# Kernel optimization log

Hardware: AMD Instinct MI355X
Metric: run time of the kernel (lower is better)

## Reference

```python
import jax, jax.numpy as jnp
import numpy as np

N = 100000   # nodes
E = 1600000  # edges (avg degree 16)
D = 128      # in_dim == out_dim (residual path)
NEG_SLOPE = 0.1


def setup_inputs() -> dict:
    key = jax.random.key(0)
    k1, k2, k3 = jax.random.split(key, 3)
    x = jax.random.normal(k1, (N, D), dtype=jnp.float32)
    edge_index = jax.random.randint(k2, (2, E), 0, N, dtype=jnp.int32)
    # GCNConv linear weight (stored as [in, out]; PyG uses x @ W^T with [out, in] — same math)
    W = jax.random.normal(k3, (D, D), dtype=jnp.float32) / np.sqrt(D).astype(np.float32)
    b = jnp.zeros((D,), dtype=jnp.float32)
    return {"x": x, "edge_index": edge_index, "W": W, "b": b}


def reference(x, edge_index, W, b):
    n = x.shape[0]
    # add self loops (GCNConv add_self_loops=True)
    loops = jnp.arange(n, dtype=edge_index.dtype)
    src = jnp.concatenate([edge_index[0], loops])
    dst = jnp.concatenate([edge_index[1], loops])
    # symmetric normalization: deg computed on destination index (PyG gcn_norm)
    deg = jax.ops.segment_sum(jnp.ones_like(dst, dtype=x.dtype), dst, num_segments=n)
    dinv = jnp.where(deg > 0, jax.lax.rsqrt(deg), 0.0)
    norm = dinv[src] * dinv[dst]                     # [E+N]
    # transform-then-propagate: small GEMM, then gather/scale/scatter
    h = x @ W                                        # [N, D]
    msgs = h[src] * norm[:, None]                    # [E+N, D] gather + scale
    agg = jax.ops.segment_sum(msgs, dst, num_segments=n) + b  # scatter-add
    act = jnp.where(agg >= 0, agg, NEG_SLOPE * agg)  # leaky_relu(0.1)
    return act + x                                   # residual (in_dim == out_dim)
```

## Files before the change

### kernel.cpp

```cpp
#include <hip/hip_runtime.h>
#include <hip/hip_bf16.h>

#define D 128
#define NEG_SLOPE 0.1f
#define BSHIFT 7
#define BSIZE 128
#define SRCBITS 17
#define SRCMASK 0x1FFFF
#define NBMAX 784
#define REGION 2432
#define EPBS 4096

typedef __attribute__((ext_vector_type(8))) short bf16x8;
typedef __attribute__((ext_vector_type(4))) float f32x4;
typedef __attribute__((ext_vector_type(2))) float f32x2;

__device__ inline unsigned short f2bf(float f) {
    unsigned u = __builtin_bit_cast(unsigned, f);
    u += 0x7fff + ((u >> 16) & 1);
    return (unsigned short)(u >> 16);
}

__global__ __launch_bounds__(256) void k_pre(const float* __restrict__ x, const float* __restrict__ W,
                                             const int* __restrict__ src, const int* __restrict__ dst,
                                             int* __restrict__ cursor, int* __restrict__ ebuf,
                                             unsigned char* __restrict__ h,
                                             int E, int NB, int n) {
    __shared__ __align__(16) unsigned char lds_u[34816];
    int b = blockIdx.x;
    int t = threadIdx.x;

    if (b < NB) {
        unsigned short* Wl = (unsigned short*)lds_u;
        const float4* W4 = (const float4*)W;
#pragma unroll
        for (int j = 0; j < 16; j++) {
            int e4 = j * 256 + t;
            float4 w = W4[e4];
            int e = e4 * 4;
            int k = e >> 7, n0 = e & 127;
            Wl[(n0 + 0) * 136 + k] = f2bf(w.x);
            Wl[(n0 + 1) * 136 + k] = f2bf(w.y);
            Wl[(n0 + 2) * 136 + k] = f2bf(w.z);
            Wl[(n0 + 3) * 136 + k] = f2bf(w.w);
        }
        __syncthreads();

        int lane = t & 63, wave = t >> 6;
        int quad = lane >> 4, mrow = lane & 15;
        int rbase = b * 128 + wave * 32;

        const float4* x4 = (const float4*)x;
        float4 a0[2][4], a1[2][4];
#pragma unroll
        for (int rt = 0; rt < 2; rt++) {
            int row = rbase + rt * 16 + mrow;
            long rowl = (row < n) ? row : (n - 1);
#pragma unroll
            for (int ks = 0; ks < 4; ks++) {
                long base = rowl * 32 + ks * 8 + quad * 2;
                a0[rt][ks] = x4[base];
                a1[rt][ks] = x4[base + 1];
            }
        }
        bf16x8 af[2][4];
#pragma unroll
        for (int rt = 0; rt < 2; rt++)
#pragma unroll
            for (int ks = 0; ks < 4; ks++) {
                bf16x8 f;
                f[0] = (short)f2bf(a0[rt][ks].x); f[1] = (short)f2bf(a0[rt][ks].y);
                f[2] = (short)f2bf(a0[rt][ks].z); f[3] = (short)f2bf(a0[rt][ks].w);
                f[4] = (short)f2bf(a1[rt][ks].x); f[5] = (short)f2bf(a1[rt][ks].y);
                f[6] = (short)f2bf(a1[rt][ks].z); f[7] = (short)f2bf(a1[rt][ks].w);
                af[rt][ks] = f;
            }

        f32x4 acc[2][8];
#pragma unroll
        for (int rt = 0; rt < 2; rt++)
#pragma unroll
            for (int ct = 0; ct < 8; ct++) acc[rt][ct] = (f32x4){0.f, 0.f, 0.f, 0.f};

#pragma unroll
        for (int ks = 0; ks < 4; ks++) {
#pragma unroll
            for (int ct = 0; ct < 8; ct++) {
                bf16x8 bf = *(bf16x8*)&Wl[(ct * 16 + mrow) * 136 + ks * 32 + quad * 8];
#pragma unroll
                for (int rt = 0; rt < 2; rt++)
                    acc[rt][ct] = __builtin_amdgcn_mfma_f32_16x16x32_bf16(af[rt][ks], bf, acc[rt][ct], 0, 0, 0);
            }
        }

#pragma unroll
        for (int rt = 0; rt < 2; rt++) {
#pragma unroll
            for (int reg = 0; reg < 4; reg++) {
                int row = rbase + rt * 16 + quad * 4 + reg;
                if (row < n) {
                    int w0 = __builtin_amdgcn_cvt_pk_fp8_f32(acc[rt][0][reg], acc[rt][1][reg], 0, false);
                    w0 = __builtin_amdgcn_cvt_pk_fp8_f32(acc[rt][2][reg], acc[rt][3][reg], w0, true);
                    int w1 = __builtin_amdgcn_cvt_pk_fp8_f32(acc[rt][4][reg], acc[rt][5][reg], 0, false);
                    w1 = __builtin_amdgcn_cvt_pk_fp8_f32(acc[rt][6][reg], acc[rt][7][reg], w1, true);
                    uint2 wv; wv.x = (unsigned)w0; wv.y = (unsigned)w1;
                    *(uint2*)&h[(long)row * 128 + mrow * 8] = wv;
                }
            }
        }
        return;
    }

    int sb = b - NB;
    int* cntL = (int*)lds_u;
    int* baseL = cntL + NBMAX;
    int* curL = baseL + NBMAX;
    for (int i = t; i < NB; i += 256) { cntL[i] = 0; }
    __syncthreads();

    const int4* src4 = (const int4*)src;
    const int4* dst4 = (const int4*)dst;
    int sv[16], dv[16];
#pragma unroll
    for (int j = 0; j < 4; j++) {
        int i4 = sb * 1024 + j * 256 + t;
        int e = i4 * 4;
        int4 s, d;
        if (e + 4 <= E) {
            s = src4[i4];
            d = dst4[i4];
        } else {
            s.x = (e < E) ? src[e] : 0;         d.x = (e < E) ? dst[e] : -1;
            s.y = (e + 1 < E) ? src[e + 1] : 0; d.y = (e + 1 < E) ? dst[e + 1] : -1;
            s.z = (e + 2 < E) ? src[e + 2] : 0; d.z = (e + 2 < E) ? dst[e + 2] : -1;
            s.w = (e + 3 < E) ? src[e + 3] : 0; d.w = (e + 3 < E) ? dst[e + 3] : -1;
        }
        sv[j * 4 + 0] = s.x; sv[j * 4 + 1] = s.y; sv[j * 4 + 2] = s.z; sv[j * 4 + 3] = s.w;
        dv[j * 4 + 0] = d.x; dv[j * 4 + 1] = d.y; dv[j * 4 + 2] = d.z; dv[j * 4 + 3] = d.w;
    }
#pragma unroll
    for (int k = 0; k < 16; k++)
        if (dv[k] >= 0) atomicAdd(&cntL[dv[k] >> BSHIFT], 1);
    __syncthreads();
    for (int i = t; i < NB; i += 256) {
        int c = cntL[i];
        if (c) baseL[i] = atomicAdd(&cursor[i], c);
        curL[i] = 0;
    }
    __syncthreads();
#pragma unroll
    for (int k = 0; k < 16; k++) {
        int d = dv[k];
        if (d >= 0) {
            int bk = d >> BSHIFT;
            int slot = baseL[bk] + atomicAdd(&curL[bk], 1);
            if (slot < REGION)
                ebuf[(long)bk * REGION + slot] = ((d & (BSIZE - 1)) << SRCBITS) | sv[k];
        }
    }
}

__global__ __launch_bounds__(256) void k_csr(const int* __restrict__ cursor, const int* __restrict__ ebuf,
                                             int* __restrict__ startA, int* __restrict__ degA,
                                             float* __restrict__ dinvA, int* __restrict__ sorted_src,
                                             int N) {
    __shared__ int srcL[REGION];
    __shared__ int cntL[BSIZE], startL[BSIZE], curL[BSIZE];

    int b = blockIdx.x, t = threadIdx.x;
    long estart = (long)b * REGION;
    int ecnt = cursor[b];
    if (ecnt > REGION) ecnt = REGION;

    if (t < BSIZE) cntL[t] = 0;
    __syncthreads();

    int ev[10];
#pragma unroll
    for (int k = 0; k < 10; k++) {
        int e = t + k * 256;
        ev[k] = (e < ecnt) ? ebuf[estart + e] : -1;
    }
#pragma unroll
    for (int k = 0; k < 10; k++)
        if (ev[k] >= 0) atomicAdd(&cntL[ev[k] >> SRCBITS], 1);
    __syncthreads();

    if (t < 64) {
        int d0 = cntL[2 * t], d1 = cntL[2 * t + 1];
        int sum = d0 + d1;
        int inc = sum;
        for (int sh = 1; sh < 64; sh <<= 1) {
            int y = __shfl_up(inc, sh, 64);
            if (t >= sh) inc += y;
        }
        int e0 = inc - sum;
        startL[2 * t] = e0;
        startL[2 * t + 1] = e0 + d0;
        curL[2 * t] = e0;
        curL[2 * t + 1] = e0 + d0;
    }
    __syncthreads();

    if (t < BSIZE) {
        int i = b * BSIZE + t;
        if (i < N) {
            startA[i] = b * REGION + startL[t];
            degA[i] = cntL[t];
            dinvA[i] = rsqrtf((float)cntL[t] + 1.0f);
        }
    }

#pragma unroll
    for (int k = 0; k < 10; k++)
        if (ev[k] >= 0) {
            int v = ev[k];
            int pos = atomicAdd(&curL[v >> SRCBITS], 1);
            srcL[pos] = v & SRCMASK;
        }
    __syncthreads();

    for (int e = t; e < ecnt; e += 256) sorted_src[estart + e] = srcL[e];
}

#define ACCVS(v, s)                                                           \
    {                                                                         \
        acc2[0] += __builtin_amdgcn_cvt_pk_f32_fp8((int)(v).x, false) * (s);  \
        acc2[1] += __builtin_amdgcn_cvt_pk_f32_fp8((int)(v).x, true) * (s);   \
        acc2[2] += __builtin_amdgcn_cvt_pk_f32_fp8((int)(v).y, false) * (s);  \
        acc2[3] += __builtin_amdgcn_cvt_pk_f32_fp8((int)(v).y, true) * (s);   \
        acc2[4] += __builtin_amdgcn_cvt_pk_f32_fp8((int)(v).z, false) * (s);  \
        acc2[5] += __builtin_amdgcn_cvt_pk_f32_fp8((int)(v).z, true) * (s);   \
        acc2[6] += __builtin_amdgcn_cvt_pk_f32_fp8((int)(v).w, false) * (s);  \
        acc2[7] += __builtin_amdgcn_cvt_pk_f32_fp8((int)(v).w, true) * (s);   \
    }

__global__ __launch_bounds__(256) void k_aggregate(const uint4* __restrict__ h4, const float* __restrict__ x,
                                                   const float* __restrict__ bias,
                                                   const int* __restrict__ startA, const int* __restrict__ degA,
                                                   const float* __restrict__ dinvA,
                                                   const int* __restrict__ sorted_src,
                                                   float* __restrict__ out, int n) {
    int wave = threadIdx.x >> 6, lane = threadIdx.x & 63;
    int i = blockIdx.x * 4 + wave;
    if (i >= n) return;
    int slot = lane >> 3, chunk = lane & 7;
    int start = startA[i], m = degA[i];
    float di = rsqrtf((float)m + 1.0f);

    f32x2 acc2[8];
#pragma unroll
    for (int r = 0; r < 8; r++) acc2[r] = (f32x2){0.f, 0.f};
    if (slot == 0) {
        uint4 v = h4[(long)i * 8 + chunk];
        ACCVS(v, di);
    }

    int j0 = 0;
    if (m >= 16) {
        int ja = start + slot;
        int e0 = sorted_src[ja], e1 = sorted_src[ja + 8];
        float dv0 = dinvA[e0], dv1 = dinvA[e1];
        for (;;) {
            uint4 v0 = h4[(long)e0 * 8 + chunk];
            uint4 v1 = h4[(long)e1 * 8 + chunk];
            j0 += 16;
            bool more = (j0 + 16 <= m);
            if (more) {
                int jb = start + j0 + slot;
                e0 = sorted_src[jb];
                e1 = sorted_src[jb + 8];
            }
            ACCVS(v0, dv0);
            ACCVS(v1, dv1);
            if (!more) break;
            dv0 = dinvA[e0];
            dv1 = dinvA[e1];
        }
    }
    if (j0 + 8 <= m) {
        int e = sorted_src[start + j0 + slot];
        float dv = dinvA[e];
        uint4 v = h4[(long)e * 8 + chunk];
        ACCVS(v, dv);
        j0 += 8;
    }
    for (int j = j0 + slot; j < m; j += 8) {
        int e = sorted_src[start + j];
        float dv = dinvA[e];
        uint4 v = h4[(long)e * 8 + chunk];
        ACCVS(v, dv);
    }

#pragma unroll
    for (int r = 0; r < 8; r++) {
        acc2[r].x += __shfl_xor(acc2[r].x, 8, 64);
        acc2[r].x += __shfl_xor(acc2[r].x, 16, 64);
        acc2[r].x += __shfl_xor(acc2[r].x, 32, 64);
        acc2[r].y += __shfl_xor(acc2[r].y, 8, 64);
        acc2[r].y += __shfl_xor(acc2[r].y, 16, 64);
        acc2[r].y += __shfl_xor(acc2[r].y, 32, 64);
    }

    int s1 = slot >> 1;
    f32x2 eL = (s1 == 0) ? acc2[0] : (s1 == 1) ? acc2[1] : (s1 == 2) ? acc2[2] : acc2[3];
    f32x2 eH = (s1 == 0) ? acc2[4] : (s1 == 1) ? acc2[5] : (s1 == 2) ? acc2[6] : acc2[7];
    float ax = (slot & 1) ? eL.y : eL.x;
    float ay = (slot & 1) ? eH.y : eH.x;

    int dbase = slot * 16 + chunk * 2;
    float2 bb = *(const float2*)&bias[dbase];
    float2 xv = *(const float2*)&x[(long)i * D + dbase];
    ax = ax * di + bb.x;
    ay = ay * di + bb.y;
    ax = (ax >= 0.f) ? ax : NEG_SLOPE * ax;
    ay = (ay >= 0.f) ? ay : NEG_SLOPE * ay;
    float2 o;
    o.x = ax + xv.x;
    o.y = ay + xv.y;
    *(float2*)&out[(long)i * D + dbase] = o;
}

extern "C" void kernel_launch(void* const* d_in, const int* in_sizes, int n_in,
                              void* d_out, int out_size, void* d_ws, size_t ws_size,
                              hipStream_t stream) {
    const float* x = (const float*)d_in[0];
    const int* edge_index = (const int*)d_in[1];
    const float* W = (const float*)d_in[2];
    const float* bias = (const float*)d_in[3];
    float* out = (float*)d_out;

    int N = in_sizes[0] / D;
    int E = in_sizes[1] / 2;
    const int* src = edge_index;
    const int* dst = edge_index + E;
    int NB = (N + BSIZE - 1) >> BSHIFT;
    int nbE = (E + EPBS - 1) / EPBS;

    char* ws = (char*)d_ws;
    size_t off = 0;
    auto alloc = [&](size_t bytes) {
        void* p = ws + off;
        off += (bytes + 15) & ~(size_t)15;
        return p;
    };
    int* cursor = (int*)alloc((size_t)NB * 4);
    int* ebuf = (int*)alloc((size_t)NB * REGION * 4);
    int* startA = (int*)alloc((size_t)N * 4);
    int* degA = (int*)alloc((size_t)N * 4);
    float* dinvA = (float*)alloc((size_t)N * 4);
    int* sorted_src = (int*)alloc((size_t)NB * REGION * 4);
    unsigned char* h = (unsigned char*)alloc((size_t)N * D);

    hipMemsetAsync(cursor, 0, (size_t)NB * 4, stream);
    k_pre<<<NB + nbE, 256, 0, stream>>>(x, W, src, dst, cursor, ebuf, h, E, NB, N);
    k_csr<<<NB, 256, 0, stream>>>(cursor, ebuf, startA, degA, dinvA, sorted_src, N);
    k_aggregate<<<(N + 3) / 4, 256, 0, stream>>>((const uint4*)h, x, bias, startA, degA, dinvA, sorted_src, out, N);
}
```

Before: 199.3 us.

## Stage bucketed edges in LDS for coalesced writes; split CSR build into half-buckets

In the edge-bucketing part of k_pre, edges are now locally sorted by bucket in LDS using a block-wide prefix scan. They are then written to ebuf in contiguous runs per bucket, replacing scattered per-edge global stores. k_csr launches two blocks per 128-node bucket, each handling 64 destinations with per-wave counters to reduce LDS atomic contention and double parallelism. The cost is extra LDS usage, more scan logic, and a per-half capacity cap (HCAP) that can silently drop edges if a half-bucket overflows.

```diff
diff --git a/kernel.cpp b/kernel.cpp
--- a/kernel.cpp
+++ b/kernel.cpp
@@ -8,8 +8,10 @@
 #define SRCBITS 17
 #define SRCMASK 0x1FFFF
 #define NBMAX 784
+#define NBPAD 1024
 #define REGION 2432
 #define EPBS 4096
+#define HCAP 1536
 
 typedef __attribute__((ext_vector_type(8))) short bf16x8;
 typedef __attribute__((ext_vector_type(4))) float f32x4;
@@ -26,7 +28,9 @@
                                              int* __restrict__ cursor, int* __restrict__ ebuf,
                                              unsigned char* __restrict__ h,
                                              int E, int NB, int n) {
-    __shared__ __align__(16) unsigned char lds_u[34816];
+    __shared__ __align__(16) unsigned char lds_u[36864];
+    __shared__ int wsum[4];
+    __shared__ int totS;
     int b = blockIdx.x;
     int t = threadIdx.x;
 
@@ -112,10 +116,13 @@
     }
 
     int sb = b - NB;
-    int* cntL = (int*)lds_u;
-    int* baseL = cntL + NBMAX;
-    int* curL = baseL + NBMAX;
-    for (int i = t; i < NB; i += 256) { cntL[i] = 0; }
+    int* cnt = (int*)lds_u;
+    int* cur = cnt + NBPAD;
+    int* delta = cur + NBPAD;
+    int* stage = delta + NBPAD;
+    unsigned short* bkt = (unsigned short*)(stage + EPBS);
+
+    for (int i = t; i < NBPAD; i += 256) cnt[i] = 0;
     __syncthreads();
 
     const int4* src4 = (const int4*)src;
@@ -140,39 +147,76 @@
     }
 #pragma unroll
     for (int k = 0; k < 16; k++)
-        if (dv[k] >= 0) atomicAdd(&cntL[dv[k] >> BSHIFT], 1);
-    __syncthreads();
-    for (int i = t; i < NB; i += 256) {
-        int c = cntL[i];
-        if (c) baseL[i] = atomicAdd(&cursor[i], c);
-        curL[i] = 0;
-    }
-    __syncthreads();
+        if (dv[k] >= 0) atomicAdd(&cnt[dv[k] >> BSHIFT], 1);
+    __syncthreads();
+
+    {
+        int lane = t & 63, wave = t >> 6;
+        int b4 = 4 * t;
+        int c0 = cnt[b4], c1 = cnt[b4 + 1], c2 = cnt[b4 + 2], c3 = cnt[b4 + 3];
+        int sum = c0 + c1 + c2 + c3;
+        int inc = sum;
+        for (int sh = 1; sh < 64; sh <<= 1) {
+            int y = __shfl_up(inc, sh, 64);
+            if (lane >= sh) inc += y;
+        }
+        if (lane == 63) wsum[wave] = inc;
+        __syncthreads();
+        int woff = 0;
+        for (int w = 0; w < wave; w++) woff += wsum[w];
+        int lb0 = woff + inc - sum;
+        int lb1 = lb0 + c0, lb2 = lb1 + c1, lb3 = lb2 + c2;
+        cur[b4] = lb0; cur[b4 + 1] = lb1; cur[b4 + 2] = lb2; cur[b4 + 3] = lb3;
+        if (c0 > 0) delta[b4] = b4 * REGION + atomicAdd(&cursor[b4], c0) - lb0;
+        if (c1 > 0) delta[b4 + 1] = (b4 + 1) * REGION + atomicAdd(&cursor[b4 + 1], c1) - lb1;
+        if (c2 > 0) delta[b4 + 2] = (b4 + 2) * REGION + atomicAdd(&cursor[b4 + 2], c2) - lb2;
+        if (c3 > 0) delta[b4 + 3] = (b4 + 3) * REGION + atomicAdd(&cursor[b4 + 3], c3) - lb3;
+        if (t == 255) totS = wsum[0] + wsum[1] + wsum[2] + wsum[3];
+    }
+    __syncthreads();
+
 #pragma unroll
     for (int k = 0; k < 16; k++) {
         int d = dv[k];
         if (d >= 0) {
             int bk = d >> BSHIFT;
-            int slot = baseL[bk] + atomicAdd(&curL[bk], 1);
-            if (slot < REGION)
-                ebuf[(long)bk * REGION + slot] = ((d & (BSIZE - 1)) << SRCBITS) | sv[k];
+            int p = atomicAdd(&cur[bk], 1);
+            stage[p] = ((d & (BSIZE - 1)) << SRCBITS) | sv[k];
+            bkt[p] = (unsigned short)bk;
+        }
+    }
+    __syncthreads();
+
+    int tot = totS;
+#pragma unroll
+    for (int j = 0; j < 16; j++) {
+        int p = j * 256 + t;
+        if (p < tot) {
+            int v = stage[p];
+            int bk = bkt[p];
+            int abs = delta[bk] + p;
+            if (abs < (bk + 1) * REGION)
+                ebuf[abs] = v;
         }
     }
 }
 
 __global__ __launch_bounds__(256) void k_csr(const int* __restrict__ cursor, const int* __restrict__ ebuf,
                                              int* __restrict__ startA, int* __restrict__ degA,
-                                             float* __restrict__ dinvA, int* __restrict__ sorted_src,
+                                             float* __restrict__ dinvA, int* __restrict__ sorted2,
                                              int N) {
-    __shared__ int srcL[REGION];
-    __shared__ int cntL[BSIZE], startL[BSIZE], curL[BSIZE];
-
-    int b = blockIdx.x, t = threadIdx.x;
+    __shared__ int srcL[HCAP];
+    __shared__ int cnt[4][64];
+    __shared__ int cur[4][64];
+    __shared__ int startL[64];
+
+    int b = blockIdx.x >> 1, half = blockIdx.x & 1;
+    int t = threadIdx.x, wave = t >> 6, lane = t & 63;
     long estart = (long)b * REGION;
     int ecnt = cursor[b];
     if (ecnt > REGION) ecnt = REGION;
 
-    if (t < BSIZE) cntL[t] = 0;
+    cnt[wave][lane] = 0;
     __syncthreads();
 
     int ev[10];
@@ -183,44 +227,49 @@
     }
 #pragma unroll
     for (int k = 0; k < 10; k++)
-        if (ev[k] >= 0) atomicAdd(&cntL[ev[k] >> SRCBITS], 1);
+        if (ev[k] >= 0) {
+            int dl = ev[k] >> SRCBITS;
+            if ((dl >> 6) == half) atomicAdd(&cnt[wave][dl & 63], 1);
+        }
     __syncthreads();
 
     if (t < 64) {
-        int d0 = cntL[2 * t], d1 = cntL[2 * t + 1];
-        int sum = d0 + d1;
-        int inc = sum;
+        int c0 = cnt[0][t], c1 = cnt[1][t], c2 = cnt[2][t], c3 = cnt[3][t];
+        int tot = c0 + c1 + c2 + c3;
+        int inc = tot;
         for (int sh = 1; sh < 64; sh <<= 1) {
             int y = __shfl_up(inc, sh, 64);
             if (t >= sh) inc += y;
         }
-        int e0 = inc - sum;
-        startL[2 * t] = e0;
-        startL[2 * t + 1] = e0 + d0;
-        curL[2 * t] = e0;
-        curL[2 * t + 1] = e0 + d0;
-    }
-    __syncthreads();
-
-    if (t < BSIZE) {
-        int i = b * BSIZE + t;
+        int st = inc - tot;
+        startL[t] = st;
+        cur[0][t] = st;
+        cur[1][t] = st + c0;
+        cur[2][t] = st + c0 + c1;
+        cur[3][t] = st + c0 + c1 + c2;
+        int i = (b << BSHIFT) + (half << 6) + t;
         if (i < N) {
-            startA[i] = b * REGION + startL[t];
-            degA[i] = cntL[t];
-            dinvA[i] = rsqrtf((float)cntL[t] + 1.0f);
-        }
-    }
+            startA[i] = blockIdx.x * HCAP + st;
+            degA[i] = tot;
+            dinvA[i] = rsqrtf((float)tot + 1.0f);
+        }
+    }
+    __syncthreads();
 
 #pragma unroll
     for (int k = 0; k < 10; k++)
         if (ev[k] >= 0) {
-            int v = ev[k];
-            int pos = atomicAdd(&curL[v >> SRCBITS], 1);
-            srcL[pos] = v & SRCMASK;
-        }
-    __syncthreads();
-
-    for (int e = t; e < ecnt; e += 256) sorted_src[estart + e] = srcL[e];
+            int dl = ev[k] >> SRCBITS;
+            if ((dl >> 6) == half) {
+                int pos = atomicAdd(&cur[wave][dl & 63], 1);
+                if (pos < HCAP) srcL[pos] = ev[k] & SRCMASK;
+            }
+        }
+    __syncthreads();
+
+    int tot = startL[63] + cnt[0][63] + cnt[1][63] + cnt[2][63] + cnt[3][63];
+    if (tot > HCAP) tot = HCAP;
+    for (int e = t; e < tot; e += 256) sorted2[(long)blockIdx.x * HCAP + e] = srcL[e];
 }
 
 #define ACCVS(v, s)                                                           \
@@ -349,11 +398,11 @@
     int* startA = (int*)alloc((size_t)N * 4);
     int* degA = (int*)alloc((size_t)N * 4);
     float* dinvA = (float*)alloc((size_t)N * 4);
-    int* sorted_src = (int*)alloc((size_t)NB * REGION * 4);
+    int* sorted2 = (int*)alloc((size_t)NB * 2 * HCAP * 4);
     unsigned char* h = (unsigned char*)alloc((size_t)N * D);
 
     hipMemsetAsync(cursor, 0, (size_t)NB * 4, stream);
     k_pre<<<NB + nbE, 256, 0, stream>>>(x, W, src, dst, cursor, ebuf, h, E, NB, N);
-    k_csr<<<NB, 256, 0, stream>>>(cursor, ebuf, startA, degA, dinvA, sorted_src, N);
-    k_aggregate<<<(N + 3) / 4, 256, 0, stream>>>((const uint4*)h, x, bias, startA, degA, dinvA, sorted_src, out, N);
+    k_csr<<<NB * 2, 256, 0, stream>>>(cursor, ebuf, startA, degA, dinvA, sorted2, N);
+    k_aggregate<<<(N + 3) / 4, 256, 0, stream>>>((const uint4*)h, x, bias, startA, degA, dinvA, sorted2, out, N);
 }
```

Result: slower. 219.3 us (+10.0%).
